# Optimization experiments

Hardware: AMD Instinct MI355X
Metric: run time of the kernel (lower is better)

## Reference

```python
import jax, jax.numpy as jnp
import numpy as np

B, T, C, H, D = 128, 256, 384, 6, 64  # batch, seq (block_size), embed, heads, head_size


def setup_inputs() -> dict:
    key = jax.random.key(0)
    ks = jax.random.split(key, 6)
    s = 0.02  # init scale
    return {
        "x": jax.random.normal(ks[0], (B, T, C), dtype=jnp.float32),
        "wq": jax.random.normal(ks[1], (H, C, D), dtype=jnp.float32) * s,
        "wk": jax.random.normal(ks[2], (H, C, D), dtype=jnp.float32) * s,
        "wv": jax.random.normal(ks[3], (H, C, D), dtype=jnp.float32) * s,
        "wp": jax.random.normal(ks[4], (H * D, C), dtype=jnp.float32) * s,
        "bp": jax.random.normal(ks[5], (C,), dtype=jnp.float32) * s,
    }


def reference(x, wq, wk, wv, wp, bp):
    # Batched multi-head causal self-attention (eval mode: dropout = identity).
    Bx, Tx, Cx = x.shape
    q = jnp.einsum("btc,hcd->bhtd", x, wq)
    k = jnp.einsum("btc,hcd->bhtd", x, wk)
    v = jnp.einsum("btc,hcd->bhtd", x, wv)
    scale = jnp.asarray(D, x.dtype) ** -0.5
    scores = jnp.einsum("bhtd,bhsd->bhts", q, k) * scale
    mask = jnp.tril(jnp.ones((Tx, Tx), dtype=bool))  # causal
    scores = jnp.where(mask, scores, -jnp.inf)
    w = jax.nn.softmax(scores, axis=-1)
    out = jnp.einsum("bhts,bhsd->bhtd", w, v)
    out = out.transpose(0, 2, 1, 3).reshape(Bx, Tx, H * D)  # concat heads
    return out @ wp + bp
```

## Files before the change

### kernel.cpp

```cpp
#include <hip/hip_runtime.h>
#include <hip/hip_bf16.h>

typedef __bf16 bf16x8 __attribute__((ext_vector_type(8)));
typedef __bf16 bf16x4 __attribute__((ext_vector_type(4)));
typedef float  f32x4  __attribute__((ext_vector_type(4)));
typedef int    i32x4  __attribute__((ext_vector_type(4)));

#define MFMA16(a,b,c) __builtin_amdgcn_mfma_f32_16x16x32_bf16((a),(b),(c),0,0,0)

static constexpr int Tt = 256;
static constexpr int Cc = 384;
static constexpr int Hh = 6;
static constexpr int Dd = 64;
static constexpr int HD = 384;
static constexpr int NQ = 1152;

__device__ __forceinline__ void gload16(const void* g, void* l) {
  __builtin_amdgcn_global_load_lds(
      (const __attribute__((address_space(1))) void*)g,
      (__attribute__((address_space(3))) void*)l, 16, 0, 0);
}

__global__ __launch_bounds__(256) void xcast(
    const float* __restrict__ x, __bf16* __restrict__ xb)
{
  size_t i = (size_t)blockIdx.x * 256 + threadIdx.x;
  const float4* p = (const float4*)(x + i * 8);
  float4 a = p[0], b = p[1];
  bf16x8 o;
  o[0] = (__bf16)a.x; o[1] = (__bf16)a.y; o[2] = (__bf16)a.z; o[3] = (__bf16)a.w;
  o[4] = (__bf16)b.x; o[5] = (__bf16)b.y; o[6] = (__bf16)b.z; o[7] = (__bf16)b.w;
  *(bf16x8*)(xb + i * 8) = o;
}

__global__ __launch_bounds__(256) void prep_w(
    const float* __restrict__ wq, const float* __restrict__ wk,
    const float* __restrict__ wv, const float* __restrict__ wp,
    __bf16* __restrict__ wqkvb, __bf16* __restrict__ wpb)
{
  int idx = blockIdx.x * 256 + threadIdx.x;
  const int n1 = NQ * Cc;
  if (idx < n1) {
    int n = idx / Cc, c = idx % Cc;
    int which = n / HD, r = n % HD, h = r >> 6, d = r & 63;
    const float* w = which == 0 ? wq : (which == 1 ? wk : wv);
    wqkvb[idx] = (__bf16)w[(h * Cc + c) * Dd + d];
  } else {
    int j = idx - n1;
    if (j < Cc * HD) {
      int co = j / HD, ci = j % HD;
      wpb[j] = (__bf16)wp[ci * Cc + co];
    }
  }
}

__global__ __launch_bounds__(256) void gemm_qkv(
    const __bf16* __restrict__ xb, const __bf16* __restrict__ wn,
    __bf16* __restrict__ qkv, int Mc)
{
  __shared__ __align__(16) char smem[36864];
  char* Al = smem;
  char* Bl = smem + 16384;

  const int tid = threadIdx.x;
  const int m0 = blockIdx.x * 128;
  const int n0 = blockIdx.y * 128;
  const int wid = tid >> 6, ln = tid & 63;
  const int wm = wid >> 1, wn_ = wid & 1;
  const int lr = ln & 15, lg = ln >> 4;
  const int srow = ln >> 3, sslot = ln & 7;

  f32x4 acc[4][4];
#pragma unroll
  for (int i = 0; i < 4; ++i)
#pragma unroll
    for (int j = 0; j < 4; ++j) acc[i][j] = f32x4{0.f, 0.f, 0.f, 0.f};

  for (int kt = 0; kt < Cc; kt += 64) {
#pragma unroll
    for (int i = 0; i < 4; ++i) {
      int off = (wid * 4 + i) << 10;
      int row = (off >> 7) + srow;
      gload16(xb + (size_t)(m0 + row) * Cc + kt + ((sslot ^ (row & 7)) << 3), Al + off);
    }
#pragma unroll
    for (int i = 0; i < 4; ++i) {
      int off = (wid * 4 + i) << 10;
      int row = (off >> 7) + srow;
      gload16(wn + (size_t)(n0 + row) * Cc + kt + ((sslot ^ (row & 7)) << 3), Bl + off);
    }
    __syncthreads();
#pragma unroll
    for (int ks = 0; ks < 2; ++ks) {
      bf16x8 af[4], bfr[4];
#pragma unroll
      for (int mi = 0; mi < 4; ++mi) {
        int r = wm * 64 + mi * 16 + lr;
        af[mi] = *(const bf16x8*)(Al + r * 128 + (((ks * 4 + lg) ^ (r & 7)) << 4));
      }
#pragma unroll
      for (int ni = 0; ni < 4; ++ni) {
        int r = wn_ * 64 + ni * 16 + lr;
        bfr[ni] = *(const bf16x8*)(Bl + r * 128 + (((ks * 4 + lg) ^ (r & 7)) << 4));
      }
      __builtin_amdgcn_s_setprio(1);
#pragma unroll
      for (int mi = 0; mi < 4; ++mi)
#pragma unroll
        for (int ni = 0; ni < 4; ++ni)
          acc[mi][ni] = MFMA16(af[mi], bfr[ni], acc[mi][ni]);
      __builtin_amdgcn_s_setprio(0);
    }
    __syncthreads();
  }

  __bf16* Cl = (__bf16*)smem;
#pragma unroll
  for (int mi = 0; mi < 4; ++mi)
#pragma unroll
    for (int ni = 0; ni < 4; ++ni)
#pragma unroll
      for (int j = 0; j < 4; ++j) {
        int row = wm * 64 + mi * 16 + lg * 4 + j;
        int col = wn_ * 64 + ni * 16 + lr;
        *((__bf16*)((char*)Cl + row * 272 + col * 2)) = (__bf16)acc[mi][ni][j];
      }
  __syncthreads();
#pragma unroll
  for (int p = 0; p < 8; ++p) {
    int row = p * 16 + (tid >> 4);
    int ch = tid & 15;
    bf16x8 v = *(const bf16x8*)((char*)Cl + row * 272 + ch * 16);
    int m = m0 + row, n = n0 + ch * 8;
    int which = n / HD, r = n % HD, h = r >> 6, d = r & 63;
    int bl = m >> 8, t = m & 255;
    *(bf16x8*)(qkv + (size_t)which * ((size_t)Mc * HD) +
               ((size_t)(bl * Hh + h) * Tt + t) * Dd + d) = v;
  }
}

__global__ __launch_bounds__(512) void attn_k(
    const __bf16* __restrict__ q, const __bf16* __restrict__ k,
    const __bf16* __restrict__ v, __bf16* __restrict__ att)
{
  __shared__ __align__(128) char smem[65536];
  char* Kl = smem;
  char* Vl = smem + 32768;

  const int bh = blockIdx.x;
  const int tid = threadIdx.x, wid = tid >> 6, lane = tid & 63;
  const int lr = lane & 15, lg = lane >> 4;
  const size_t base = (size_t)bh * (Tt * Dd);

#pragma unroll
  for (int i = 0; i < 4; ++i) {
    int off = (wid * 4 + i) << 10;
    int row = (off >> 7) + (lane >> 3);
    int slot = lane & 7;
    gload16(k + base + row * 64 + ((slot ^ (row & 7)) << 3), Kl + off);
  }
#pragma unroll
  for (int i = 0; i < 4; ++i) {
    int chunk = tid + 512 * i;
    int key = chunk >> 3, d8 = chunk & 7;
    bf16x8 vv = *(const bf16x8*)(v + base + key * 64 + d8 * 8);
#pragma unroll
    for (int e = 0; e < 8; ++e) {
      int d = d8 * 8 + e;
      *(__bf16*)(Vl + ((d * 512 + key * 2) ^ ((d & 7) << 4))) = vv[e];
    }
  }
  __syncthreads();

  const int bl = bh / Hh, h = bh % Hh;

  for (int qi = 0; qi < 2; ++qi) {
    const int qt = (qi == 0) ? wid : 15 - wid;
    const int qbase = qt * 16;

    bf16x8 qf0 = *(const bf16x8*)(q + base + (qbase + lr) * 64 + lg * 8);
    bf16x8 qf1 = *(const bf16x8*)(q + base + (qbase + lr) * 64 + 32 + lg * 8);

    f32x4 s[16];
#pragma unroll
    for (int n = 0; n < 16; ++n) s[n] = f32x4{0.f, 0.f, 0.f, 0.f};
    __builtin_amdgcn_s_setprio(1);
#pragma unroll
    for (int n = 0; n < 16; ++n) {
      if (n <= qt) {
        int rowb = (n * 16 + lr) * 128;
        int swz = (lr & 7) << 4;
        bf16x8 k0 = *(const bf16x8*)(Kl + ((rowb + lg * 16) ^ swz));
        bf16x8 k1 = *(const bf16x8*)(Kl + ((rowb + 64 + lg * 16) ^ swz));
        s[n] = MFMA16(k0, qf0, s[n]);
        s[n] = MFMA16(k1, qf1, s[n]);
      }
    }
    __builtin_amdgcn_s_setprio(0);

    float mx = -1e30f;
#pragma unroll
    for (int n = 0; n < 16; ++n) {
      if (n <= qt) {
#pragma unroll
        for (int j = 0; j < 4; ++j) {
          float sv = s[n][j] * 0.125f;
          if (n == qt && 4 * lg + j > lr) sv = -1e30f;
          s[n][j] = sv;
          mx = fmaxf(mx, sv);
        }
      }
    }
    mx = fmaxf(mx, __shfl_xor(mx, 16));
    mx = fmaxf(mx, __shfl_xor(mx, 32));

    float sum = 0.f;
    int w[16][2];
#pragma unroll
    for (int n = 0; n < 16; ++n) {
      if (n <= qt) {
        float e0 = __expf(s[n][0] - mx);
        float e1 = __expf(s[n][1] - mx);
        float e2 = __expf(s[n][2] - mx);
        float e3 = __expf(s[n][3] - mx);
        sum += (e0 + e1) + (e2 + e3);
        union { __bf16 hh[2]; int ii; } u0, u1;
        u0.hh[0] = (__bf16)e0; u0.hh[1] = (__bf16)e1;
        u1.hh[0] = (__bf16)e2; u1.hh[1] = (__bf16)e3;
        w[n][0] = u0.ii;
        w[n][1] = u1.ii;
      } else if (n == (qt | 1)) {
        w[n][0] = 0; w[n][1] = 0;
      }
    }
    sum += __shfl_xor(sum, 16);
    sum += __shfl_xor(sum, 32);
    float inv = 1.0f / sum;

    f32x4 o[4];
#pragma unroll
    for (int dn = 0; dn < 4; ++dn) o[dn] = f32x4{0.f, 0.f, 0.f, 0.f};
    const int kkmax = qt >> 1;
#pragma unroll
    for (int kk = 0; kk < 8; ++kk) {
      if (kk <= kkmax) {
        int s0 = lr + ((lg & 1) << 5);
        int s1 = s0 + 16;
        int hi = lg >> 1;
        int a0 = __shfl(w[2 * kk][0], s0), b0 = __shfl(w[2 * kk + 1][0], s0);
        int a1 = __shfl(w[2 * kk][1], s0), b1 = __shfl(w[2 * kk + 1][1], s0);
        int a2 = __shfl(w[2 * kk][0], s1), b2 = __shfl(w[2 * kk + 1][0], s1);
        int a3 = __shfl(w[2 * kk][1], s1), b3 = __shfl(w[2 * kk + 1][1], s1);
        i32x4 pwv;
        pwv[0] = hi ? b0 : a0;
        pwv[1] = hi ? b1 : a1;
        pwv[2] = hi ? b2 : a2;
        pwv[3] = hi ? b3 : a3;
        bf16x8 pa = __builtin_bit_cast(bf16x8, pwv);

        __builtin_amdgcn_s_setprio(1);
#pragma unroll
        for (int dn = 0; dn < 4; ++dn) {
          int d = dn * 16 + lr;
          bf16x8 vb = *(const bf16x8*)(Vl + ((d * 512 + kk * 64 + lg * 16) ^ ((d & 7) << 4)));
          o[dn] = MFMA16(pa, vb, o[dn]);
        }
        __builtin_amdgcn_s_setprio(0);
      }
    }

#pragma unroll
    for (int j = 0; j < 4; ++j) {
      float invj = __shfl(inv, lg * 4 + j, 16);
      int qrow = qbase + lg * 4 + j;
#pragma unroll
      for (int dn = 0; dn < 4; ++dn)
        att[((size_t)(bl * Tt + qrow)) * HD + h * Dd + dn * 16 + lr] =
            (__bf16)(o[dn][j] * invj);
    }
  }
}

__global__ __launch_bounds__(256) void gemm_out(
    const __bf16* __restrict__ att, const __bf16* __restrict__ wpb,
    const float* __restrict__ bp, float* __restrict__ out, int Mc)
{
  __shared__ __align__(16) char smem[32768];
  char* Al = smem;
  char* Bl = smem + 16384;

  const int tid = threadIdx.x;
  const int m0 = blockIdx.x * 128;
  const int n0 = blockIdx.y * 128;
  const int wid = tid >> 6, ln = tid & 63;
  const int wm = wid >> 1, wn_ = wid & 1;
  const int lr = ln & 15, lg = ln >> 4;
  const int srow = ln >> 3, sslot = ln & 7;

  f32x4 acc[4][4];
#pragma unroll
  for (int i = 0; i < 4; ++i)
#pragma unroll
    for (int j = 0; j < 4; ++j) acc[i][j] = f32x4{0.f, 0.f, 0.f, 0.f};

  for (int kt = 0; kt < Cc; kt += 64) {
#pragma unroll
    for (int i = 0; i < 4; ++i) {
      int off = (wid * 4 + i) << 10;
      int row = (off >> 7) + srow;
      gload16(att + (size_t)(m0 + row) * Cc + kt + ((sslot ^ (row & 7)) << 3), Al + off);
    }
#pragma unroll
    for (int i = 0; i < 4; ++i) {
      int off = (wid * 4 + i) << 10;
      int row = (off >> 7) + srow;
      gload16(wpb + (size_t)(n0 + row) * Cc + kt + ((sslot ^ (row & 7)) << 3), Bl + off);
    }
    __syncthreads();
#pragma unroll
    for (int ks = 0; ks < 2; ++ks) {
      bf16x8 af[4], bfr[4];
#pragma unroll
      for (int mi = 0; mi < 4; ++mi) {
        int r = wm * 64 + mi * 16 + lr;
        af[mi] = *(const bf16x8*)(Al + r * 128 + (((ks * 4 + lg) ^ (r & 7)) << 4));
      }
#pragma unroll
      for (int ni = 0; ni < 4; ++ni) {
        int r = wn_ * 64 + ni * 16 + lr;
        bfr[ni] = *(const bf16x8*)(Bl + r * 128 + (((ks * 4 + lg) ^ (r & 7)) << 4));
      }
      __builtin_amdgcn_s_setprio(1);
#pragma unroll
      for (int mi = 0; mi < 4; ++mi)
#pragma unroll
        for (int ni = 0; ni < 4; ++ni)
          acc[mi][ni] = MFMA16(af[mi], bfr[ni], acc[mi][ni]);
      __builtin_amdgcn_s_setprio(0);
    }
    __syncthreads();
  }
#pragma unroll
  for (int ni = 0; ni < 4; ++ni) {
    int n = n0 + wn_ * 64 + ni * 16 + lr;
    float bv = bp[n];
#pragma unroll
    for (int mi = 0; mi < 4; ++mi)
#pragma unroll
      for (int j = 0; j < 4; ++j) {
        int m = m0 + wm * 64 + mi * 16 + lg * 4 + j;
        out[(size_t)m * Cc + n] = acc[mi][ni][j] + bv;
      }
  }
}

extern "C" void kernel_launch(void* const* d_in, const int* in_sizes, int n_in,
                              void* d_out, int out_size, void* d_ws, size_t ws_size,
                              hipStream_t stream) {
  const float* x  = (const float*)d_in[0];
  const float* wq = (const float*)d_in[1];
  const float* wk = (const float*)d_in[2];
  const float* wv = (const float*)d_in[3];
  const float* wp = (const float*)d_in[4];
  const float* bp = (const float*)d_in[5];
  float* out = (float*)d_out;

  char* ws = (char*)d_ws;
  __bf16* wqkvb = (__bf16*)ws;
  __bf16* wpb   = (__bf16*)(ws + 884736);
  char*   dyn   = ws + 1179648;

  int Bc = 128;
  while (Bc > 1 && 1179648ull + (unsigned long long)Bc * 786432ull > (unsigned long long)ws_size)
    Bc >>= 1;
  const int Mc = Bc * 256;
  __bf16* xb  = (__bf16*)dyn;
  __bf16* att = xb;
  __bf16* qkv = (__bf16*)(dyn + (size_t)Mc * HD * 2);

  prep_w<<<2304, 256, 0, stream>>>(wq, wk, wv, wp, wqkvb, wpb);

  for (int b0 = 0; b0 < 128; b0 += Bc) {
    const float* xc  = x + (size_t)b0 * Tt * Cc;
    float* outc      = out + (size_t)b0 * Tt * Cc;
    xcast<<<Bc * 48, 256, 0, stream>>>(xc, xb);
    gemm_qkv<<<dim3(Mc / 128, 9), 256, 0, stream>>>(xb, wqkvb, qkv, Mc);
    attn_k<<<Bc * Hh, 512, 0, stream>>>(qkv, qkv + (size_t)Mc * HD,
                                        qkv + (size_t)2 * Mc * HD, att);
    gemm_out<<<dim3(Mc / 128, 3), 256, 0, stream>>>(att, wpb, bp, outc, Mc);
  }
}
```

Before: 208.2 us.

## Double-buffer LDS staging in both GEMMs and tile-transpose weight prep

Both bf16 GEMMs now use two 32KB LDS buffers, issuing global-to-LDS loads for the next K tile while computing on the current one, so load latency is meant to overlap with MFMA work. The weight prep kernel is rewritten as 64x64 tiled transposes through shared memory with vectorized stores, replacing scattered per-element gathers. The doubled LDS footprint (64KB per block) may lower occupancy. The loop tail shown does not reveal whether a barrier guards the buffer reuse, which risks a race.

New measurement: 203.3 us. 1.02x faster.

```diff
diff --git a/kernel.cpp b/kernel.cpp
--- a/kernel.cpp
+++ b/kernel.cpp
@@ -19,6 +19,18 @@
   __builtin_amdgcn_global_load_lds(
       (const __attribute__((address_space(1))) void*)g,
       (__attribute__((address_space(3))) void*)l, 16, 0, 0);
+}
+
+__device__ __forceinline__ void stage_ab(const __bf16* a, const __bf16* b,
+                                         char* lbase, int wid, int srow, int sslot) {
+#pragma unroll
+  for (int i = 0; i < 4; ++i) {
+    int loff = (wid * 4 + i) << 10;
+    int row = (loff >> 7) + srow;
+    int co = (sslot ^ (row & 7)) << 3;
+    gload16(a + (size_t)row * Cc + co, lbase + loff);
+    gload16(b + (size_t)row * Cc + co, lbase + 16384 + loff);
+  }
 }
 
 __global__ __launch_bounds__(256) void xcast(
@@ -33,24 +45,38 @@
   *(bf16x8*)(xb + i * 8) = o;
 }
 
-__global__ __launch_bounds__(256) void prep_w(
+__global__ __launch_bounds__(256) void prep_w2(
     const float* __restrict__ wq, const float* __restrict__ wk,
     const float* __restrict__ wv, const float* __restrict__ wp,
     __bf16* __restrict__ wqkvb, __bf16* __restrict__ wpb)
 {
-  int idx = blockIdx.x * 256 + threadIdx.x;
-  const int n1 = NQ * Cc;
-  if (idx < n1) {
-    int n = idx / Cc, c = idx % Cc;
-    int which = n / HD, r = n % HD, h = r >> 6, d = r & 63;
-    const float* w = which == 0 ? wq : (which == 1 ? wk : wv);
-    wqkvb[idx] = (__bf16)w[(h * Cc + c) * Dd + d];
+  __shared__ __bf16 t[64][72];
+  const int b = blockIdx.x, tid = threadIdx.x;
+  const float* src; __bf16* dst;
+  int row0, col0, rs, dr0, dc0;
+  if (b < 108) {
+    int which = b / 36, rem = b % 36, h = rem / 6, ct = rem % 6;
+    src = which == 0 ? wq : (which == 1 ? wk : wv);
+    row0 = h * 384 + ct * 64; col0 = 0; rs = 64;
+    dst = wqkvb; dr0 = which * 384 + h * 64; dc0 = ct * 64;
   } else {
-    int j = idx - n1;
-    if (j < Cc * HD) {
-      int co = j / HD, ci = j % HD;
-      wpb[j] = (__bf16)wp[ci * Cc + co];
-    }
+    int b2 = b - 108, rt = b2 / 6, ct2 = b2 % 6;
+    src = wp; row0 = ct2 * 64; col0 = rt * 64; rs = 384;
+    dst = wpb; dr0 = rt * 64; dc0 = ct2 * 64;
+  }
+  const int tr = tid >> 6, tc = tid & 63;
+#pragma unroll
+  for (int i = 0; i < 16; ++i) {
+    int r = i * 4 + tr;
+    t[tc][r] = (__bf16)src[(size_t)(row0 + r) * rs + col0 + tc];
+  }
+  __syncthreads();
+#pragma unroll
+  for (int i = 0; i < 2; ++i) {
+    int chunk = tid + 256 * i;
+    int r = chunk >> 3, c8 = chunk & 7;
+    bf16x8 v = *(const bf16x8*)&t[r][c8 * 8];
+    *(bf16x8*)(dst + (size_t)(dr0 + r) * 384 + dc0 + c8 * 8) = v;
   }
 }
 
@@ -58,9 +84,7 @@
     const __bf16* __restrict__ xb, const __bf16* __restrict__ wn,
     __bf16* __restrict__ qkv, int Mc)
 {
-  __shared__ __align__(16) char smem[36864];
-  char* Al = smem;
-  char* Bl = smem + 16384;
+  __shared__ __align__(16) char smem[65536];
 
   const int tid = threadIdx.x;
   const int m0 = blockIdx.x * 128;
@@ -70,26 +94,25 @@
   const int lr = ln & 15, lg = ln >> 4;
   const int srow = ln >> 3, sslot = ln & 7;
 
+  const __bf16* a0 = xb + (size_t)m0 * Cc;
+  const __bf16* b0 = wn + (size_t)n0 * Cc;
+
   f32x4 acc[4][4];
 #pragma unroll
   for (int i = 0; i < 4; ++i)
 #pragma unroll
     for (int j = 0; j < 4; ++j) acc[i][j] = f32x4{0.f, 0.f, 0.f, 0.f};
 
-  for (int kt = 0; kt < Cc; kt += 64) {
-#pragma unroll
-    for (int i = 0; i < 4; ++i) {
-      int off = (wid * 4 + i) << 10;
-      int row = (off >> 7) + srow;
-      gload16(xb + (size_t)(m0 + row) * Cc + kt + ((sslot ^ (row & 7)) << 3), Al + off);
-    }
-#pragma unroll
-    for (int i = 0; i < 4; ++i) {
-      int off = (wid * 4 + i) << 10;
-      int row = (off >> 7) + srow;
-      gload16(wn + (size_t)(n0 + row) * Cc + kt + ((sslot ^ (row & 7)) << 3), Bl + off);
-    }
-    __syncthreads();
+  stage_ab(a0, b0, smem, wid, srow, sslot);
+  __syncthreads();
+#pragma unroll
+  for (int t = 0; t < 6; ++t) {
+    const int base = (t & 1) * 32768;
+    if (t < 5)
+      stage_ab(a0 + (t + 1) * 64, b0 + (t + 1) * 64,
+               smem + (((t + 1) & 1) * 32768), wid, srow, sslot);
+    char* Al = smem + base;
+    char* Bl = smem + base + 16384;
 #pragma unroll
     for (int ks = 0; ks < 2; ++ks) {
       bf16x8 af[4], bfr[4];
@@ -285,9 +308,7 @@
     const __bf16* __restrict__ att, const __bf16* __restrict__ wpb,
     const float* __restrict__ bp, float* __restrict__ out, int Mc)
 {
-  __shared__ __align__(16) char smem[32768];
-  char* Al = smem;
-  char* Bl = smem + 16384;
+  __shared__ __align__(16) char smem[65536];
 
   const int tid = threadIdx.x;
   const int m0 = blockIdx.x * 128;
@@ -297,26 +318,25 @@
   const int lr = ln & 15, lg = ln >> 4;
   const int srow = ln >> 3, sslot = ln & 7;
 
+  const __bf16* a0 = att + (size_t)m0 * Cc;
+  const __bf16* b0 = wpb + (size_t)n0 * Cc;
+
   f32x4 acc[4][4];
 #pragma unroll
   for (int i = 0; i < 4; ++i)
 #pragma unroll
     for (int j = 0; j < 4; ++j) acc[i][j] = f32x4{0.f, 0.f, 0.f, 0.f};
 
-  for (int kt = 0; kt < Cc; kt += 64) {
-#pragma unroll
-    for (int i = 0; i < 4; ++i) {
-      int off = (wid * 4 + i) << 10;
-      int row = (off >> 7) + srow;
-      gload16(att + (size_t)(m0 + row) * Cc + kt + ((sslot ^ (row & 7)) << 3), Al + off);
-    }
-#pragma unroll
-    for (int i = 0; i < 4; ++i) {
-      int off = (wid * 4 + i) << 10;
-      int row = (off >> 7) + srow;
-      gload16(wpb + (size_t)(n0 + row) * Cc + kt + ((sslot ^ (row & 7)) << 3), Bl + off);
-    }
-    __syncthreads();
+  stage_ab(a0, b0, smem, wid, srow, sslot);
+  __syncthreads();
+#pragma unroll
+  for (int t = 0; t < 6; ++t) {
+    const int base = (t & 1) * 32768;
+    if (t < 5)
+      stage_ab(a0 + (t + 1) * 64, b0 + (t + 1) * 64,
+               smem + (((t + 1) & 1) * 32768), wid, srow, sslot);
+    char* Al = smem + base;
+    char* Bl = smem + base + 16384;
 #pragma unroll
     for (int ks = 0; ks < 2; ++ks) {
       bf16x8 af[4], bfr[4];
@@ -378,7 +398,7 @@
   __bf16* att = xb;
   __bf16* qkv = (__bf16*)(dyn + (size_t)Mc * HD * 2);
 
-  prep_w<<<2304, 256, 0, stream>>>(wq, wk, wv, wp, wqkvb, wpb);
+  prep_w2<<<144, 256, 0, stream>>>(wq, wk, wv, wp, wqkvb, wpb);
 
   for (int b0 = 0; b0 < 128; b0 += Bc) {
     const float* xc  = x + (size_t)b0 * Tt * Cc;
```
